# Optimization experiments

Measured on AMD Instinct MI355X. Metric: run time of the kernel, lower is better.

## Reference

```python
import jax, jax.numpy as jnp
import numpy as np

B, C, T, L, H = 4, 512, 8, 512, 8


def _normalize(a, eps=1e-12):
    # F.normalize: x / max(||x||_2, eps) along last dim
    n = jnp.linalg.norm(a, axis=-1, keepdims=True)
    return a / jnp.maximum(n, eps)


def setup_inputs() -> dict:
    key = jax.random.key(0)
    ks = jax.random.split(key, 8)
    w = lambda k, shp: (jax.random.normal(k, shp, dtype=jnp.float32) * 0.02)
    return {
        "e": jax.random.normal(ks[0], (B, C, T, L), dtype=jnp.float32),
        "x": jax.random.normal(ks[1], (B, C, T, L), dtype=jnp.float32),
        "Wq": w(ks[2], (C, C)), "bq": jnp.zeros((C,), jnp.float32),
        "Wkv": w(ks[3], (2 * C, C)), "bkv": jnp.zeros((2 * C,), jnp.float32),
        "Wm": w(ks[4], (C, C)), "bm": jnp.zeros((C,), jnp.float32),
        "Wg1": w(ks[5], (C, C)), "bg1": jnp.zeros((C,), jnp.float32),
        "Wg2": w(ks[6], (H, C)), "bg2": jnp.zeros((H,), jnp.float32),
    }


def reference(e, x, Wq, bq, Wkv, bkv, Wm, bm, Wg1, bg1, Wg2, bg2):
    shortcut = x
    xp = jnp.transpose(x, (0, 2, 3, 1))  # (b,t,l,c)
    ep = jnp.transpose(e, (0, 2, 3, 1))  # (b,t,l,c)
    b, t, l, c = xp.shape
    hd = c // H

    # per-(b,t) head gating from pooled e (gate_weights1 == gate_weights in source)
    pooled = ep.mean(axis=2)  # (b,t,c)
    glog = jnp.tanh(pooled @ Wg1.T + bg1) @ Wg2.T + bg2  # (b,t,H)
    gw = jax.nn.softmax(glog, axis=-1)[..., None, None]  # (b,t,H,1,1)

    q = (ep @ Wq.T + bq).reshape(b, t, l, H, hd).transpose(0, 1, 3, 2, 4)  # (b,t,H,l,hd)
    q = _normalize(q)
    kv = (xp @ Wkv.T + bkv).reshape(b, t, l, 2 * H, hd).transpose(0, 1, 3, 2, 4)
    k, v = kv[:, :, :H], kv[:, :, H:]
    k = _normalize(k)
    v = _normalize(v) * gw  # pre-softmax value gating

    scale = jnp.float32(1.0 / np.sqrt(hd))
    att = jax.nn.softmax(jnp.einsum('bthid,bthjd->bthij', q, k) * scale, axis=-1)
    o = jnp.einsum('bthij,bthjd->bthid', att, v) * gw  # post-attention gating

    o = o.transpose(0, 1, 3, 2, 4).reshape(b, t, l, c)
    o = o @ Wm.T + bm
    return jnp.transpose(o, (0, 3, 1, 2)) + shortcut
```

## Files before the change

kernel.cpp:

```cpp
#include <hip/hip_runtime.h>
#include <math.h>

#define B_ 4
#define C_ 512
#define T_ 8
#define L_ 512
#define H_ 8
#define HD_ 64

typedef unsigned short ushort_t;
using short8 = __attribute__((ext_vector_type(8))) short;
using f4 = __attribute__((ext_vector_type(4))) float;

#define GLOAD_LDS(gp, lp)                                                      \
  __builtin_amdgcn_global_load_lds(                                            \
      (const __attribute__((address_space(1))) unsigned int*)(gp),             \
      (__attribute__((address_space(3))) unsigned int*)(lp), 16, 0, 0)

__device__ __forceinline__ unsigned pack_bf16(float a, float b) {
  union { float f; unsigned u; } ua, ub;
  ua.f = a; ub.f = b;
  unsigned ra = (ua.u + 0x7FFFu + ((ua.u >> 16) & 1u)) >> 16;
  unsigned rb = (ub.u + 0x7FFFu + ((ub.u >> 16) & 1u)) >> 16;
  return (rb << 16) | (ra & 0xFFFFu);
}
__device__ __forceinline__ ushort_t bf16_1(float a) {
  union { float f; unsigned u; } ua; ua.f = a;
  return (ushort_t)((ua.u + 0x7FFFu + ((ua.u >> 16) & 1u)) >> 16);
}


__global__ __launch_bounds__(256) void gate1_kernel(const float* __restrict__ pooled,
                                                    const float* __restrict__ Wg1,
                                                    const float* __restrict__ bg1,
                                                    float* __restrict__ h1) {
  int w = threadIdx.x >> 6, lane = threadIdx.x & 63;
  int row = blockIdx.x * 4 + w;
  int bt = blockIdx.y;
  const float* wr = Wg1 + (size_t)row * C_;
  const float* pr = pooled + bt * C_;
  float s = 0.f;
#pragma unroll
  for (int i = 0; i < 8; ++i) s += wr[lane + i * 64] * pr[lane + i * 64];
#pragma unroll
  for (int off = 32; off > 0; off >>= 1) s += __shfl_down(s, off, 64);
  if (lane == 0) h1[bt * C_ + row] = tanhf(s + bg1[row]);
}

__global__ __launch_bounds__(256) void gate2_kernel(const float* __restrict__ h1,
                                                    const float* __restrict__ Wg2,
                                                    const float* __restrict__ bg2,
                                                    float* __restrict__ gwp) {
  __shared__ float part[256];
  __shared__ float gl[H_];
  int bt = blockIdx.x, tid = threadIdx.x;
  int h = tid >> 5, s = tid & 31;
  const float* w2 = Wg2 + (size_t)h * C_;
  const float* hb = h1 + bt * C_;
  float p = 0.f;
  for (int c = s; c < C_; c += 32) p += w2[c] * hb[c];
  part[tid] = p;
  __syncthreads();
  if (tid < H_) {
    float a = bg2[tid];
    for (int i = 0; i < 32; ++i) a += part[tid * 32 + i];
    gl[tid] = a;
  }
  __syncthreads();
  if (tid == 0) {
    float m = -1e30f;
    for (int i = 0; i < H_; ++i) m = fmaxf(m, gl[i]);
    float sum = 0.f;
    float ex[H_];
    for (int i = 0; i < H_; ++i) { ex[i] = expf(gl[i] - m); sum += ex[i]; }
    for (int i = 0; i < H_; ++i) gwp[bt * H_ + i] = ex[i] / sum;
  }
}

__global__ __launch_bounds__(256) void cvt_kernel(const float* __restrict__ s,
                                                  ushort_t* __restrict__ d) {
  int i = (blockIdx.x * 256 + threadIdx.x) * 8;
  float4 a = *(const float4*)(s + i);
  float4 b = *(const float4*)(s + i + 4);
  uint4 o;
  o.x = pack_bf16(a.x, a.y); o.y = pack_bf16(a.z, a.w);
  o.z = pack_bf16(b.x, b.y); o.w = pack_bf16(b.z, b.w);
  *(uint4*)(d + i) = o;
}

__global__ __launch_bounds__(256) void tconv_kernel(const float* __restrict__ src,
                                                    ushort_t* __restrict__ dst,
                                                    float* __restrict__ pooled) {
  __shared__ float tb[64][65];
  int tid = threadIdx.x;
  int b = blockIdx.z >> 3, t = blockIdx.z & 7;
  int c0 = blockIdx.y * 64, l0 = blockIdx.x * 64;
  const float* sp = src + (((size_t)(b * C_ + c0) * T_) + t) * L_ + l0;
  int j = tid & 63, i0 = tid >> 6;
#pragma unroll
  for (int p = 0; p < 16; ++p) {
    int i = p * 4 + i0;
    tb[i][j] = sp[(size_t)i * (T_ * L_) + j];
  }
  __syncthreads();
  if (pooled) {
    int c = tid >> 2, part = tid & 3;
    float s = 0.f;
#pragma unroll
    for (int k = 0; k < 16; ++k) s += tb[c][part * 16 + k];
    s += __shfl_down(s, 1);
    s += __shfl_down(s, 2);
    if (part == 0) atomicAdd(&pooled[blockIdx.z * C_ + c0 + c], s * (1.0f / L_));
  }
  int ii = (tid & 31) * 2, jj0 = tid >> 5;
  ushort_t* dp = dst + ((size_t)blockIdx.z * L_ + l0) * C_ + c0;
#pragma unroll
  for (int p = 0; p < 8; ++p) {
    int jj = p * 8 + jj0;
    *(unsigned*)(dp + (size_t)jj * C_ + ii) = pack_bf16(tb[ii][jj], tb[ii + 1][jj]);
  }
}

__global__ __launch_bounds__(256, 2) void gemm_mfma(
    const ushort_t* __restrict__ Aq, const ushort_t* __restrict__ BTq,
    const float* __restrict__ biasq, const ushort_t* __restrict__ Akv,
    const ushort_t* __restrict__ BTkv, const float* __restrict__ biaskv,
    int mode, float* __restrict__ Out, const float* __restrict__ resid,
    ushort_t* __restrict__ Qdst, ushort_t* __restrict__ Kdst,
    ushort_t* __restrict__ Vdst, const float* __restrict__ gwp) {
  __shared__ alignas(16) ushort_t As[128 * 32];
  __shared__ alignas(16) ushort_t Bs[128 * 32];
  int tid = threadIdx.x;
  int w = tid >> 6, lane = tid & 63, l15 = lane & 15, q = lane >> 4;
  int n0 = blockIdx.x * 128, bt = blockIdx.z;
  int wm = (w >> 1) * 64, wn = (w & 1) * 64;

  const ushort_t* A;
  const ushort_t* BT;
  const float* bias;
  int m0, lmode;
  if (mode == 3) {
    if (blockIdx.y < 4) {
      A = Aq; BT = BTq; bias = biasq; lmode = 1; m0 = blockIdx.y * 128;
    } else {
      A = Akv; BT = BTkv; bias = biaskv; lmode = 2; m0 = (blockIdx.y - 4) * 128;
    }
  } else {
    A = Aq; BT = BTq; bias = biasq; lmode = 0; m0 = blockIdx.y * 128;
  }
  const ushort_t* Bbt = BT + (size_t)bt * C_ * C_;

  int c0 = w * 64 + lane, c1 = 256 + w * 64 + lane;
  const ushort_t* ag0 = A + (size_t)(m0 + (c0 >> 2)) * 512 + (c0 & 3) * 8;
  const ushort_t* ag1 = A + (size_t)(m0 + (c1 >> 2)) * 512 + (c1 & 3) * 8;
  const ushort_t* bg0 = Bbt + (size_t)(n0 + (c0 >> 2)) * 512 + (c0 & 3) * 8;
  const ushort_t* bg1 = Bbt + (size_t)(n0 + (c1 >> 2)) * 512 + (c1 & 3) * 8;
  ushort_t* la0 = As + (size_t)(w * 64) * 8;
  ushort_t* la1 = As + (size_t)(256 + w * 64) * 8;
  ushort_t* lb0 = Bs + (size_t)(w * 64) * 8;
  ushort_t* lb1 = Bs + (size_t)(256 + w * 64) * 8;

  f4 acc[4][4];
#pragma unroll
  for (int i = 0; i < 4; ++i)
#pragma unroll
    for (int j = 0; j < 4; ++j) acc[i][j] = (f4){0.f, 0.f, 0.f, 0.f};

  for (int k0 = 0; k0 < 512; k0 += 32) {
    __syncthreads();
    GLOAD_LDS(ag0 + k0, la0);
    GLOAD_LDS(ag1 + k0, la1);
    GLOAD_LDS(bg0 + k0, lb0);
    GLOAD_LDS(bg1 + k0, lb1);
    __syncthreads();
    short8 af[4], bf[4];
#pragma unroll
    for (int mt = 0; mt < 4; ++mt)
      af[mt] = *(const short8*)&As[(size_t)(wm + mt * 16 + l15) * 32 + q * 8];
#pragma unroll
    for (int nt = 0; nt < 4; ++nt)
      bf[nt] = *(const short8*)&Bs[(size_t)(wn + nt * 16 + l15) * 32 + q * 8];
#pragma unroll
    for (int mt = 0; mt < 4; ++mt)
#pragma unroll
      for (int nt = 0; nt < 4; ++nt)
        acc[mt][nt] =
            __builtin_amdgcn_mfma_f32_16x16x32_bf16(af[mt], bf[nt], acc[mt][nt], 0, 0, 0);
  }

#pragma unroll
  for (int mt = 0; mt < 4; ++mt)
#pragma unroll
    for (int r = 0; r < 4; ++r) {
      float bb = bias[m0 + wm + mt * 16 + q * 4 + r];
#pragma unroll
      for (int nt = 0; nt < 4; ++nt) acc[mt][nt][r] += bb;
    }

  if (lmode == 0) {
    int b = bt >> 3, t = bt & 7;
    float* Ob = Out + (size_t)b * (C_ * T_ * L_) + (size_t)t * L_;
    const float* Rb = resid + (size_t)b * (C_ * T_ * L_) + (size_t)t * L_;
#pragma unroll
    for (int mt = 0; mt < 4; ++mt)
#pragma unroll
      for (int r = 0; r < 4; ++r) {
        size_t ro = (size_t)(m0 + wm + mt * 16 + q * 4 + r) * (T_ * L_);
#pragma unroll
        for (int nt = 0; nt < 4; ++nt) {
          int n = n0 + wn + nt * 16 + l15;
          Ob[ro + n] = acc[mt][nt][r] + Rb[ro + n];
        }
      }
    return;
  }

  float scale[4];
#pragma unroll
  for (int nt = 0; nt < 4; ++nt) {
    float s = 0.f;
#pragma unroll
    for (int mt = 0; mt < 4; ++mt)
#pragma unroll
      for (int r = 0; r < 4; ++r) s += acc[mt][nt][r] * acc[mt][nt][r];
    s += __shfl_xor(s, 16);
    s += __shfl_xor(s, 32);
    scale[nt] = s;
  }
  int hh = ((m0 + wm) >> 6) & 7;
  bool isv = (lmode == 2) && (m0 + wm >= 512);
  float mult = isv ? gwp[bt * H_ + hh] : (lmode == 1 ? 0.125f : 1.0f);
#pragma unroll
  for (int nt = 0; nt < 4; ++nt)
    scale[nt] = mult / fmaxf(sqrtf(scale[nt]), 1e-12f);

  if (!isv) {
    ushort_t* Db = (lmode == 1 ? Qdst : Kdst) + (size_t)(bt * H_ + hh) * 512 * 64;
#pragma unroll
    for (int nt = 0; nt < 4; ++nt) {
      int l = n0 + wn + nt * 16 + l15;
      ushort_t* rowp = Db + (size_t)l * 64;
#pragma unroll
      for (int mt = 0; mt < 4; ++mt) {
        uint2 pk;
        pk.x = pack_bf16(acc[mt][nt][0] * scale[nt], acc[mt][nt][1] * scale[nt]);
        pk.y = pack_bf16(acc[mt][nt][2] * scale[nt], acc[mt][nt][3] * scale[nt]);
        *(uint2*)&rowp[mt * 16 + q * 4] = pk;
      }
    }
  } else {
    ushort_t* Vb = Vdst + (size_t)(bt * H_ + hh) * 64 * 512;
#pragma unroll
    for (int mt = 0; mt < 4; ++mt)
#pragma unroll
      for (int r = 0; r < 4; ++r) {
        int d = mt * 16 + q * 4 + r;
        ushort_t* rp = Vb + (size_t)d * 512 + n0 + wn;
#pragma unroll
        for (int nt = 0; nt < 4; ++nt)
          rp[nt * 16 + l15] = bf16_1(acc[mt][nt][r] * scale[nt]);
      }
  }
}

__global__ __launch_bounds__(512, 4) void attn_kernel(
    const ushort_t* __restrict__ Qbf, const ushort_t* __restrict__ Kbf,
    const ushort_t* __restrict__ Vbf, const float* __restrict__ gwp,
    ushort_t* __restrict__ obfT) {
  int tid = threadIdx.x;
  int w = tid >> 6, lane = tid & 63, l15 = lane & 15, q = lane >> 4;
  int qb = blockIdx.x, h = blockIdx.y, bt = blockIdx.z;
  int iw = qb * 256 + w * 32;

  const ushort_t* Qg = Qbf + (size_t)(bt * H_ + h) * 512 * 64;
  const ushort_t* Kg = Kbf + (size_t)(bt * H_ + h) * 512 * 64;
  const ushort_t* Vg = Vbf + (size_t)(bt * H_ + h) * 64 * 512;

  short8 qf[2][2];
#pragma unroll
  for (int f = 0; f < 2; ++f) {
    const ushort_t* qrow = Qg + (size_t)(iw + f * 16 + l15) * 64;
    qf[f][0] = *(const short8*)&qrow[q * 8];
    qf[f][1] = *(const short8*)&qrow[32 + q * 8];
  }

  f4 acc[2][4];
#pragma unroll
  for (int f = 0; f < 2; ++f)
#pragma unroll
    for (int dt = 0; dt < 4; ++dt) acc[f][dt] = (f4){0.f, 0.f, 0.f, 0.f};
  float lsum[2] = {0.f, 0.f};
  bool hi_half = (lane >= 32);
  int qh2 = (q & 1) * 2;

  for (int j0 = 0; j0 < 512; j0 += 64) {
    short8 kf[4][2], vf[2][4];
#pragma unroll
    for (int jt = 0; jt < 4; ++jt) {
      const ushort_t* krow = Kg + (size_t)(j0 + jt * 16 + l15) * 64;
      kf[jt][0] = *(const short8*)&krow[q * 8];
      kf[jt][1] = *(const short8*)&krow[32 + q * 8];
    }
#pragma unroll
    for (int ks2 = 0; ks2 < 2; ++ks2)
#pragma unroll
      for (int dt = 0; dt < 4; ++dt)
        vf[ks2][dt] = *(const short8*)(Vg + (size_t)(dt * 16 + l15) * 512 + j0 +
                                       ks2 * 32 + q * 8);

#pragma unroll
    for (int f = 0; f < 2; ++f) {
      f4 sc[4];
#pragma unroll
      for (int jt = 0; jt < 4; ++jt) {
        f4 c = {0.f, 0.f, 0.f, 0.f};
        c = __builtin_amdgcn_mfma_f32_16x16x32_bf16(kf[jt][0], qf[f][0], c, 0, 0, 0);
        c = __builtin_amdgcn_mfma_f32_16x16x32_bf16(kf[jt][1], qf[f][1], c, 0, 0, 0);
        sc[jt] = c;
      }
      float ls = 0.f;
#pragma unroll
      for (int jt = 0; jt < 4; ++jt)
#pragma unroll
        for (int r = 0; r < 4; ++r) {
          float p = __expf(sc[jt][r]);
          sc[jt][r] = p;
          ls += p;
        }
      lsum[f] += ls;

      unsigned pk01[4], pk23[4];
#pragma unroll
      for (int jt = 0; jt < 4; ++jt) {
        pk01[jt] = pack_bf16(sc[jt][0], sc[jt][1]);
        pk23[jt] = pack_bf16(sc[jt][2], sc[jt][3]);
      }
#pragma unroll
      for (int ks2 = 0; ks2 < 2; ++ks2) {
        union { unsigned u[4]; short8 s; } bu;
#pragma unroll
        for (int r = 0; r < 4; ++r) {
          int src = (qh2 + (r >> 1)) * 16 + l15;
          unsigned pl = (r & 1) ? pk23[ks2 * 2] : pk01[ks2 * 2];
          unsigned ph = (r & 1) ? pk23[ks2 * 2 + 1] : pk01[ks2 * 2 + 1];
          unsigned lo = __shfl(pl, src);
          unsigned hi = __shfl(ph, src);
          bu.u[r] = hi_half ? hi : lo;
        }
#pragma unroll
        for (int dt = 0; dt < 4; ++dt)
          acc[f][dt] = __builtin_amdgcn_mfma_f32_16x16x32_bf16(vf[ks2][dt], bu.s,
                                                               acc[f][dt], 0, 0, 0);
      }
    }
  }

  float g = gwp[bt * H_ + h];
#pragma unroll
  for (int f = 0; f < 2; ++f) {
    float ls = lsum[f];
    ls += __shfl_xor(ls, 16);
    ls += __shfl_xor(ls, 32);
    float inv = g / ls;
    int iglob = iw + f * 16 + l15;
    ushort_t* ob = obfT + ((size_t)(bt * 512 + iglob)) * 512 + h * 64;
#pragma unroll
    for (int dt = 0; dt < 4; ++dt) {
      uint2 pk;
      pk.x = pack_bf16(acc[f][dt][0] * inv, acc[f][dt][1] * inv);
      pk.y = pack_bf16(acc[f][dt][2] * inv, acc[f][dt][3] * inv);
      *(uint2*)&ob[dt * 16 + q * 4] = pk;
    }
  }
}

extern "C" void kernel_launch(void* const* d_in, const int* in_sizes, int n_in,
                              void* d_out, int out_size, void* d_ws, size_t ws_size,
                              hipStream_t stream) {
  const float* e   = (const float*)d_in[0];
  const float* x   = (const float*)d_in[1];
  const float* Wq  = (const float*)d_in[2];
  const float* bq  = (const float*)d_in[3];
  const float* Wkv = (const float*)d_in[4];
  const float* bkv = (const float*)d_in[5];
  const float* Wm  = (const float*)d_in[6];
  const float* bm  = (const float*)d_in[7];
  const float* Wg1 = (const float*)d_in[8];
  const float* bg1 = (const float*)d_in[9];
  const float* Wg2 = (const float*)d_in[10];
  const float* bg2 = (const float*)d_in[11];
  float* out = (float*)d_out;

  float* ws = (float*)d_ws;
  float* pooled = ws;
  float* gwp    = ws + 16384;
  float* h1buf  = ws + 16640;
  float* fb     = ws + 33024;
  ushort_t* ebfT = (ushort_t*)(fb);
  ushort_t* xbfT = (ushort_t*)(fb + 1 * 4194304);
  ushort_t* Qbf  = (ushort_t*)(fb + 2 * 4194304);
  ushort_t* Kbf  = (ushort_t*)(fb + 3 * 4194304);
  ushort_t* Vbf  = (ushort_t*)(fb + 4 * 4194304);
  ushort_t* obfT = (ushort_t*)(fb + 5 * 4194304);
  ushort_t* Wqb  = (ushort_t*)(fb + 6 * 4194304);
  ushort_t* Wkvb = Wqb + 262144;
  ushort_t* Wmb  = Wkvb + 524288;

  hipMemsetAsync(pooled, 0, 16384 * sizeof(float), stream);
  cvt_kernel<<<dim3(128), dim3(256), 0, stream>>>(Wq, Wqb);
  cvt_kernel<<<dim3(256), dim3(256), 0, stream>>>(Wkv, Wkvb);
  cvt_kernel<<<dim3(128), dim3(256), 0, stream>>>(Wm, Wmb);
  tconv_kernel<<<dim3(8, 8, 32), dim3(256), 0, stream>>>(e, ebfT, pooled);
  tconv_kernel<<<dim3(8, 8, 32), dim3(256), 0, stream>>>(x, xbfT, nullptr);
  gate1_kernel<<<dim3(128, 32), dim3(256), 0, stream>>>(pooled, Wg1, bg1, h1buf);
  gate2_kernel<<<dim3(32), dim3(256), 0, stream>>>(h1buf, Wg2, bg2, gwp);
  gemm_mfma<<<dim3(4, 12, 32), dim3(256), 0, stream>>>(
      Wqb, ebfT, bq, Wkvb, xbfT, bkv, 3, nullptr, nullptr, Qbf, Kbf, Vbf, gwp);
  attn_kernel<<<dim3(2, H_, 32), dim3(512), 0, stream>>>(Qbf, Kbf, Vbf, gwp, obfT);
  gemm_mfma<<<dim3(4, 4, 32), dim3(256), 0, stream>>>(
      Wmb, obfT, bm, nullptr, nullptr, nullptr, 0, out, x, nullptr, nullptr,
      nullptr, gwp);
}
```

Measured before the change: 280.5 us.

## Merge conversion launches and give each attention wave more query rows with K prefetch

The three weight-conversion launches become one kernel, and the two transpose-convert launches for e and x become one. The attention kernel now has each block cover all 512 query rows of a head, with each wave handling 64 rows instead of 32. Each loaded K/V tile is therefore reused across twice as many queries, and the K tile for the next step is double-buffered in registers. In exchange, register pressure rises (launch bounds lowered to 2 blocks per CU), and there are half as many attention blocks, which may reduce latency hiding.

```diff
diff --git a/kernel.cpp b/kernel.cpp
--- a/kernel.cpp
+++ b/kernel.cpp
@@ -77,23 +77,39 @@
   }
 }
 
-__global__ __launch_bounds__(256) void cvt_kernel(const float* __restrict__ s,
-                                                  ushort_t* __restrict__ d) {
+__global__ __launch_bounds__(256) void cvt3_kernel(const float* __restrict__ Wq,
+                                                   const float* __restrict__ Wkv,
+                                                   const float* __restrict__ Wm,
+                                                   ushort_t* __restrict__ dWq,
+                                                   ushort_t* __restrict__ dWkv,
+                                                   ushort_t* __restrict__ dWm) {
   int i = (blockIdx.x * 256 + threadIdx.x) * 8;
-  float4 a = *(const float4*)(s + i);
-  float4 b = *(const float4*)(s + i + 4);
+  const float* s;
+  ushort_t* d;
+  int off;
+  if (i < 262144)      { s = Wq;  d = dWq;  off = i; }
+  else if (i < 786432) { s = Wkv; d = dWkv; off = i - 262144; }
+  else                 { s = Wm;  d = dWm;  off = i - 786432; }
+  float4 a = *(const float4*)(s + off);
+  float4 b = *(const float4*)(s + off + 4);
   uint4 o;
   o.x = pack_bf16(a.x, a.y); o.y = pack_bf16(a.z, a.w);
   o.z = pack_bf16(b.x, b.y); o.w = pack_bf16(b.z, b.w);
-  *(uint4*)(d + i) = o;
-}
-
-__global__ __launch_bounds__(256) void tconv_kernel(const float* __restrict__ src,
-                                                    ushort_t* __restrict__ dst,
+  *(uint4*)(d + off) = o;
+}
+
+__global__ __launch_bounds__(256) void tconv_kernel(const float* __restrict__ e,
+                                                    const float* __restrict__ x,
+                                                    ushort_t* __restrict__ ebfT,
+                                                    ushort_t* __restrict__ xbfT,
                                                     float* __restrict__ pooled) {
   __shared__ float tb[64][65];
   int tid = threadIdx.x;
-  int b = blockIdx.z >> 3, t = blockIdx.z & 7;
+  bool isE = blockIdx.z < 32;
+  int bt = isE ? blockIdx.z : blockIdx.z - 32;
+  const float* src = isE ? e : x;
+  ushort_t* dst = isE ? ebfT : xbfT;
+  int b = bt >> 3, t = bt & 7;
   int c0 = blockIdx.y * 64, l0 = blockIdx.x * 64;
   const float* sp = src + (((size_t)(b * C_ + c0) * T_) + t) * L_ + l0;
   int j = tid & 63, i0 = tid >> 6;
@@ -103,17 +119,17 @@
     tb[i][j] = sp[(size_t)i * (T_ * L_) + j];
   }
   __syncthreads();
-  if (pooled) {
+  if (isE) {
     int c = tid >> 2, part = tid & 3;
     float s = 0.f;
 #pragma unroll
     for (int k = 0; k < 16; ++k) s += tb[c][part * 16 + k];
     s += __shfl_down(s, 1);
     s += __shfl_down(s, 2);
-    if (part == 0) atomicAdd(&pooled[blockIdx.z * C_ + c0 + c], s * (1.0f / L_));
+    if (part == 0) atomicAdd(&pooled[bt * C_ + c0 + c], s * (1.0f / L_));
   }
   int ii = (tid & 31) * 2, jj0 = tid >> 5;
-  ushort_t* dp = dst + ((size_t)blockIdx.z * L_ + l0) * C_ + c0;
+  ushort_t* dp = dst + ((size_t)bt * L_ + l0) * C_ + c0;
 #pragma unroll
   for (int p = 0; p < 8; ++p) {
     int jj = p * 8 + jj0;
@@ -263,59 +279,71 @@
   }
 }
 
-__global__ __launch_bounds__(512, 4) void attn_kernel(
+__global__ __launch_bounds__(512, 2) void attn_kernel(
     const ushort_t* __restrict__ Qbf, const ushort_t* __restrict__ Kbf,
     const ushort_t* __restrict__ Vbf, const float* __restrict__ gwp,
     ushort_t* __restrict__ obfT) {
   int tid = threadIdx.x;
   int w = tid >> 6, lane = tid & 63, l15 = lane & 15, q = lane >> 4;
-  int qb = blockIdx.x, h = blockIdx.y, bt = blockIdx.z;
-  int iw = qb * 256 + w * 32;
+  int h = blockIdx.x, bt = blockIdx.y;
 
   const ushort_t* Qg = Qbf + (size_t)(bt * H_ + h) * 512 * 64;
   const ushort_t* Kg = Kbf + (size_t)(bt * H_ + h) * 512 * 64;
   const ushort_t* Vg = Vbf + (size_t)(bt * H_ + h) * 64 * 512;
 
-  short8 qf[2][2];
-#pragma unroll
-  for (int f = 0; f < 2; ++f) {
-    const ushort_t* qrow = Qg + (size_t)(iw + f * 16 + l15) * 64;
+  short8 qf[4][2];
+#pragma unroll
+  for (int f = 0; f < 4; ++f) {
+    const ushort_t* qrow = Qg + (size_t)(w * 64 + f * 16 + l15) * 64;
     qf[f][0] = *(const short8*)&qrow[q * 8];
     qf[f][1] = *(const short8*)&qrow[32 + q * 8];
   }
 
-  f4 acc[2][4];
-#pragma unroll
-  for (int f = 0; f < 2; ++f)
+  f4 acc[4][4];
+#pragma unroll
+  for (int f = 0; f < 4; ++f)
 #pragma unroll
     for (int dt = 0; dt < 4; ++dt) acc[f][dt] = (f4){0.f, 0.f, 0.f, 0.f};
-  float lsum[2] = {0.f, 0.f};
+  float lsum[4] = {0.f, 0.f, 0.f, 0.f};
   bool hi_half = (lane >= 32);
   int qh2 = (q & 1) * 2;
 
-  for (int j0 = 0; j0 < 512; j0 += 64) {
-    short8 kf[4][2], vf[2][4];
-#pragma unroll
-    for (int jt = 0; jt < 4; ++jt) {
-      const ushort_t* krow = Kg + (size_t)(j0 + jt * 16 + l15) * 64;
-      kf[jt][0] = *(const short8*)&krow[q * 8];
-      kf[jt][1] = *(const short8*)&krow[32 + q * 8];
-    }
+  short8 kf[2][4][2];
+#pragma unroll
+  for (int jt = 0; jt < 4; ++jt) {
+    const ushort_t* kr = Kg + (size_t)(jt * 16 + l15) * 64;
+    kf[0][jt][0] = *(const short8*)&kr[q * 8];
+    kf[0][jt][1] = *(const short8*)&kr[32 + q * 8];
+  }
+
+#pragma unroll
+  for (int jj = 0; jj < 8; ++jj) {
+    const int j0 = jj * 64;
+    const int cur = jj & 1;
+    short8 vf[2][4];
 #pragma unroll
     for (int ks2 = 0; ks2 < 2; ++ks2)
 #pragma unroll
       for (int dt = 0; dt < 4; ++dt)
         vf[ks2][dt] = *(const short8*)(Vg + (size_t)(dt * 16 + l15) * 512 + j0 +
                                        ks2 * 32 + q * 8);
-
-#pragma unroll
-    for (int f = 0; f < 2; ++f) {
+    if (jj < 7) {
+#pragma unroll
+      for (int jt = 0; jt < 4; ++jt) {
+        const ushort_t* kr = Kg + (size_t)(j0 + 64 + jt * 16 + l15) * 64;
+        kf[cur ^ 1][jt][0] = *(const short8*)&kr[q * 8];
+        kf[cur ^ 1][jt][1] = *(const short8*)&kr[32 + q * 8];
+      }
+    }
+
+#pragma unroll
+    for (int f = 0; f < 4; ++f) {
       f4 sc[4];
 #pragma unroll
       for (int jt = 0; jt < 4; ++jt) {
         f4 c = {0.f, 0.f, 0.f, 0.f};
-        c = __builtin_amdgcn_mfma_f32_16x16x32_bf16(kf[jt][0], qf[f][0], c, 0, 0, 0);
-        c = __builtin_amdgcn_mfma_f32_16x16x32_bf16(kf[jt][1], qf[f][1], c, 0, 0, 0);
+        c = __builtin_amdgcn_mfma_f32_16x16x32_bf16(kf[cur][jt][0], qf[f][0], c, 0, 0, 0);
+        c = __builtin_amdgcn_mfma_f32_16x16x32_bf16(kf[cur][jt][1], qf[f][1], c, 0, 0, 0);
         sc[jt] = c;
       }
       float ls = 0.f;
@@ -357,12 +385,12 @@
 
   float g = gwp[bt * H_ + h];
 #pragma unroll
-  for (int f = 0; f < 2; ++f) {
+  for (int f = 0; f < 4; ++f) {
     float ls = lsum[f];
     ls += __shfl_xor(ls, 16);
     ls += __shfl_xor(ls, 32);
     float inv = g / ls;
-    int iglob = iw + f * 16 + l15;
+    int iglob = w * 64 + f * 16 + l15;
     ushort_t* ob = obfT + ((size_t)(bt * 512 + iglob)) * 512 + h * 64;
 #pragma unroll
     for (int dt = 0; dt < 4; ++dt) {
@@ -407,16 +435,13 @@
   ushort_t* Wmb  = Wkvb + 524288;
 
   hipMemsetAsync(pooled, 0, 16384 * sizeof(float), stream);
-  cvt_kernel<<<dim3(128), dim3(256), 0, stream>>>(Wq, Wqb);
-  cvt_kernel<<<dim3(256), dim3(256), 0, stream>>>(Wkv, Wkvb);
-  cvt_kernel<<<dim3(128), dim3(256), 0, stream>>>(Wm, Wmb);
-  tconv_kernel<<<dim3(8, 8, 32), dim3(256), 0, stream>>>(e, ebfT, pooled);
-  tconv_kernel<<<dim3(8, 8, 32), dim3(256), 0, stream>>>(x, xbfT, nullptr);
+  cvt3_kernel<<<dim3(512), dim3(256), 0, stream>>>(Wq, Wkv, Wm, Wqb, Wkvb, Wmb);
+  tconv_kernel<<<dim3(8, 8, 64), dim3(256), 0, stream>>>(e, x, ebfT, xbfT, pooled);
   gate1_kernel<<<dim3(128, 32), dim3(256), 0, stream>>>(pooled, Wg1, bg1, h1buf);
   gate2_kernel<<<dim3(32), dim3(256), 0, stream>>>(h1buf, Wg2, bg2, gwp);
   gemm_mfma<<<dim3(4, 12, 32), dim3(256), 0, stream>>>(
       Wqb, ebfT, bq, Wkvb, xbfT, bkv, 3, nullptr, nullptr, Qbf, Kbf, Vbf, gwp);
-  attn_kernel<<<dim3(2, H_, 32), dim3(512), 0, stream>>>(Qbf, Kbf, Vbf, gwp, obfT);
+  attn_kernel<<<dim3(H_, 32), dim3(512), 0, stream>>>(Qbf, Kbf, Vbf, gwp, obfT);
   gemm_mfma<<<dim3(4, 4, 32), dim3(256), 0, stream>>>(
       Wmb, obfT, bm, nullptr, nullptr, nullptr, 0, out, x, nullptr, nullptr,
       nullptr, gwp);
```

Result: slower. 434.7 us (+55.0%).
